# Performance work log

Hardware: AMD Instinct MI355X
Metric: run time of the kernel (lower is better)

The kernel has to match this reference:

```python
import jax, jax.numpy as jnp
import numpy as np
import math

MIN_INTEGRAL = 1e-05
INTERVAL_TIME = 0.05


def setup_inputs() -> dict:
    key = jax.random.key(0)
    ks = jax.random.split(key, 8)
    B, S, U, W = 8192, 256, 128, 512  # batch, state, user_params, hidden width
    D_in = S + U
    sc = lambda fan_in: 1.0 / np.sqrt(fan_in)
    return {
        "state": jax.random.normal(ks[0], (B, S), dtype=jnp.float32),
        "user_params": jax.random.normal(ks[1], (B, U), dtype=jnp.float32),
        "W1": jax.random.normal(ks[2], (D_in, W), dtype=jnp.float32) * sc(D_in),
        "b1": jax.random.normal(ks[3], (W,), dtype=jnp.float32) * 0.01,
        "W2": jax.random.normal(ks[4], (W, W), dtype=jnp.float32) * sc(W),
        "b2": jax.random.normal(ks[5], (W,), dtype=jnp.float32) * 0.01,
        "W3": jax.random.normal(ks[6], (W, S), dtype=jnp.float32) * sc(W),
        "b3": jax.random.normal(ks[7], (S,), dtype=jnp.float32) * 0.01,
        "h": 1,
    }


def reference(state, user_params, W1, b1, W2, b2, W3, b3, h):
    # ode_func: cat(state, user_params) -> Linear -> SiLU -> Linear -> SiLU -> Linear
    def ode_func(s):
        x = jnp.concatenate((s, user_params), axis=1)
        x = jax.nn.silu(x @ W1 + b1)
        x = jax.nn.silu(x @ W2 + b2)
        return x @ W3 + b3

    num_intervals = int(math.floor(h / INTERVAL_TIME))  # fp-faithful to torch code

    def step(s, _):
        return s + ode_func(s) * INTERVAL_TIME, None

    state, _ = jax.lax.scan(step, state, None, length=num_intervals)

    rest_interval = h % INTERVAL_TIME
    if MIN_INTEGRAL < rest_interval:
        # NOTE: original code adds the derivative WITHOUT scaling by rest_interval
        state = state + ode_func(state)
    return state
```

## Files before the change

kernel.cpp:

```cpp
#include <hip/hip_runtime.h>

typedef __attribute__((ext_vector_type(8))) short short8;
typedef __attribute__((ext_vector_type(4))) float float4v;
typedef unsigned short u16;

#define Sdim 256
#define Udim 128
#define Hdim 512
#define MT   32
#define XS   392
#define XLS  264
#define HS   520
#define NW   589824
#define W1_OFF 0
#define W2_OFF 196608
#define W3_OFF 458752
#define NSTEPS 21

__device__ __forceinline__ float bf2f(u16 u) {
    union { unsigned int i; float f; } x; x.i = ((unsigned int)u) << 16; return x.f;
}
__device__ __forceinline__ u16 f2bf(float f) {
    union { float f; unsigned int i; } x; x.f = f;
    unsigned int r = x.i + 0x7FFFu + ((x.i >> 16) & 1u);
    return (u16)(r >> 16);
}

__device__ __forceinline__ int probe_local(const u16* __restrict__ w1, int tid) {
    __shared__ int cnt;
    if (tid == 0) cnt = 0;
    __syncthreads();
    if (tid < 256) {
        u16 u = w1[tid];
        int e = (u >> 7) & 0xFF;
        if ((u == 0) || (e >= 0x60 && e <= 0x8F)) atomicAdd(&cnt, 1);
    }
    __syncthreads();
    return (cnt >= 240) ? 1 : 0;
}

__device__ __forceinline__ void pack_body(const void* __restrict__ Wraw, u16* __restrict__ hi,
                                          int K, int N, int f, int bf) {
    int KT = K >> 5;
    int lane = f & 63, tile = f >> 6;
    int kt = tile % KT, nt = tile / KT;
    int k0 = kt * 32 + ((lane >> 4) << 3);
    int n  = nt * 16 + (lane & 15);
    short8 vh;
#pragma unroll
    for (int j = 0; j < 8; ++j) {
        float wv = bf ? bf2f(((const u16*)Wraw)[(size_t)(k0 + j) * N + n])
                      : ((const float*)Wraw)[(size_t)(k0 + j) * N + n];
        vh[j] = (short)f2bf(wv);
    }
    *reinterpret_cast<short8*>(hi + (size_t)f * 8) = vh;
}

__global__ void pack_all(const void* __restrict__ W1, const void* __restrict__ W2,
                         const void* __restrict__ W3, u16* __restrict__ wh,
                         int* __restrict__ flagp) {
    int bf = probe_local((const u16*)W1, threadIdx.x);
    int b = blockIdx.x;
    if (b == 0 && threadIdx.x == 0) *flagp = bf;
    if (b < 96)
        pack_body(W1, wh + W1_OFF, 384, 512, b * 256 + threadIdx.x, bf);
    else if (b < 224)
        pack_body(W2, wh + W2_OFF, 512, 512, (b - 96) * 256 + threadIdx.x, bf);
    else
        pack_body(W3, wh + W3_OFF, 512, 256, (b - 224) * 256 + threadIdx.x, bf);
}

#define MFMA __builtin_amdgcn_mfma_f32_16x16x32_bf16

template<int KT0, int KT, int KTB, int KTL, int NT>
__device__ __forceinline__ void mm1(const u16* ah, const u16* al, const int as, const int als,
                                    const u16* __restrict__ wh, float4v acc[2][NT]) {
#pragma unroll 2
    for (int kt = KT0; kt < KT; ++kt) {
        short8 A0 = *(const short8*)(ah + kt * 32);
        short8 A1 = *(const short8*)(ah + 16 * as + kt * 32);
        short8 A0l, A1l;
        if (kt < KTL) {
            A0l = *(const short8*)(al + kt * 32);
            A1l = *(const short8*)(al + 16 * als + kt * 32);
        }
#pragma unroll
        for (int t = 0; t < NT; ++t) {
            short8 Bh = *(const short8*)(wh + (size_t)(t * KTB + kt) * 512);
            acc[0][t] = MFMA(A0, Bh, acc[0][t], 0, 0, 0);
            acc[1][t] = MFMA(A1, Bh, acc[1][t], 0, 0, 0);
            if (kt < KTL) {
                acc[0][t] = MFMA(A0l, Bh, acc[0][t], 0, 0, 0);
                acc[1][t] = MFMA(A1l, Bh, acc[1][t], 0, 0, 0);
            }
        }
    }
}

__device__ __forceinline__ float silu(float v) {
    return v * __builtin_amdgcn_rcpf(1.0f + __expf(-v));
}

template<bool BF>
__device__ __forceinline__ void body(
    const void* state_raw, const void* user_raw,
    const void* b1r, const void* b2r, const void* b3r,
    const u16* __restrict__ wh_all, void* outp,
    u16* xh, u16* xl, u16* H1, u16* H2) {

    const int tid = threadIdx.x, w = tid >> 6, lane = tid & 63;
    const int col16 = lane & 15, quad = lane >> 4;
    const int r0 = blockIdx.x * MT;

    if (tid < 512) {
        int row = tid >> 4;
        int c8 = (tid & 15) * 8;
        if (BF) {
            short8 v = *(const short8*)((const u16*)user_raw + (size_t)(r0 + row) * Udim + c8);
            *(short8*)(xh + row * XS + Sdim + c8) = v;
        } else {
            const float* up = (const float*)user_raw + (size_t)(r0 + row) * Udim + c8;
            short8 v;
#pragma unroll
            for (int j = 0; j < 8; ++j) v[j] = (short)f2bf(up[j]);
            *(short8*)(xh + row * XS + Sdim + c8) = v;
        }
    }
    float b1f[2], b2f[2], b3f;
#pragma unroll
    for (int t = 0; t < 2; ++t) {
        int i = w * 32 + t * 16 + col16;
        b1f[t] = BF ? bf2f(((const u16*)b1r)[i]) : ((const float*)b1r)[i];
        b2f[t] = BF ? bf2f(((const u16*)b2r)[i]) : ((const float*)b2r)[i];
    }
    {
        int i = w * 16 + col16;
        b3f = BF ? bf2f(((const u16*)b3r)[i]) : ((const float*)b3r)[i];
    }
    float st[2][4];
#pragma unroll
    for (int m = 0; m < 2; ++m)
#pragma unroll
        for (int r = 0; r < 4; ++r) {
            int row = m * 16 + quad * 4 + r;
            int col = w * 16 + col16;
            float v = BF ? bf2f(((const u16*)state_raw)[(size_t)(r0 + row) * Sdim + col])
                         : ((const float*)state_raw)[(size_t)(r0 + row) * Sdim + col];
            st[m][r] = v;
            u16 h = f2bf(v);
            xh[row * XS + col] = h;
            xl[row * XLS + col] = f2bf(v - bf2f(h));
        }
    __syncthreads();

    const u16* w1h = wh_all + W1_OFF + (size_t)(w * 2) * 12 * 512 + lane * 8;
    const u16* w2h = wh_all + W2_OFF + (size_t)(w * 2) * 16 * 512 + lane * 8;
    const u16* w3h = wh_all + W3_OFF + (size_t)(w)     * 16 * 512 + lane * 8;

    const u16* aXh = xh + col16 * XS + quad * 8;
    const u16* aXl = xl + col16 * XLS + quad * 8;
    const u16* aH1 = H1 + col16 * HS + quad * 8;
    const u16* aH2 = H2 + col16 * HS + quad * 8;

    float4v uacc[2][2];
#pragma unroll
    for (int m = 0; m < 2; ++m)
#pragma unroll
        for (int t = 0; t < 2; ++t) uacc[m][t] = (float4v){b1f[t], b1f[t], b1f[t], b1f[t]};
    mm1<8, 12, 12, 0, 2>(aXh, aXh, XS, XS, w1h, uacc);

    for (int step = 0; step < NSTEPS; ++step) {
        const float dt = (step == NSTEPS - 1) ? 1.0f : 0.05f;
        const bool lo_now = (step == 0) || (step == NSTEPS - 1);

        {
            float4v acc[2][2];
#pragma unroll
            for (int m = 0; m < 2; ++m)
#pragma unroll
                for (int t = 0; t < 2; ++t) acc[m][t] = uacc[m][t];
            if (lo_now) mm1<0, 8, 12, 8, 2>(aXh, aXl, XS, XLS, w1h, acc);
            else        mm1<0, 8, 12, 0, 2>(aXh, aXl, XS, XLS, w1h, acc);
#pragma unroll
            for (int m = 0; m < 2; ++m)
#pragma unroll
                for (int t = 0; t < 2; ++t)
#pragma unroll
                    for (int r = 0; r < 4; ++r) {
                        float s = silu(acc[m][t][r]);
                        H1[(m * 16 + quad * 4 + r) * HS + w * 32 + t * 16 + col16] = f2bf(s);
                    }
        }
        __syncthreads();

        {
            float4v acc[2][2];
#pragma unroll
            for (int m = 0; m < 2; ++m)
#pragma unroll
                for (int t = 0; t < 2; ++t) acc[m][t] = (float4v){b2f[t], b2f[t], b2f[t], b2f[t]};
            mm1<0, 16, 16, 0, 2>(aH1, aH1, HS, HS, w2h, acc);
#pragma unroll
            for (int m = 0; m < 2; ++m)
#pragma unroll
                for (int t = 0; t < 2; ++t)
#pragma unroll
                    for (int r = 0; r < 4; ++r) {
                        float s = silu(acc[m][t][r]);
                        H2[(m * 16 + quad * 4 + r) * HS + w * 32 + t * 16 + col16] = f2bf(s);
                    }
        }
        __syncthreads();

        {
            float4v acc[2][1];
#pragma unroll
            for (int m = 0; m < 2; ++m) acc[m][0] = (float4v){b3f, b3f, b3f, b3f};
            mm1<0, 16, 16, 0, 1>(aH2, aH2, HS, HS, w3h, acc);
#pragma unroll
            for (int m = 0; m < 2; ++m)
#pragma unroll
                for (int r = 0; r < 4; ++r) {
                    float v = st[m][r] + acc[m][0][r] * dt;
                    st[m][r] = v;
                    if (step < NSTEPS - 1) {
                        int row = m * 16 + quad * 4 + r;
                        int col = w * 16 + col16;
                        u16 h = f2bf(v);
                        xh[row * XS + col] = h;
                        xl[row * XLS + col] = f2bf(v - bf2f(h));
                    }
                }
        }
        __syncthreads();
    }

#pragma unroll
    for (int m = 0; m < 2; ++m)
#pragma unroll
        for (int r = 0; r < 4; ++r) {
            int row = m * 16 + quad * 4 + r;
            int col = w * 16 + col16;
            if (BF) ((u16*)outp)[(size_t)(r0 + row) * Sdim + col] = f2bf(st[m][r]);
            else    ((float*)outp)[(size_t)(r0 + row) * Sdim + col] = st[m][r];
        }
}

__global__ __launch_bounds__(1024, 4) void fused_ode(
    const void* state_raw, const void* user_raw,
    const void* b1r, const void* b2r, const void* b3r,
    const u16* __restrict__ wh, const int* __restrict__ flagp, void* outp) {

    __shared__ __align__(16) u16 xh[MT * XS];
    __shared__ __align__(16) u16 xl[MT * XLS];
    __shared__ __align__(16) u16 H1[MT * HS];
    __shared__ __align__(16) u16 H2[MT * HS];

    if (*flagp)
        body<true >(state_raw, user_raw, b1r, b2r, b3r, wh, outp, xh, xl, H1, H2);
    else
        body<false>(state_raw, user_raw, b1r, b2r, b3r, wh, outp, xh, xl, H1, H2);
}

extern "C" void kernel_launch(void* const* d_in, const int* in_sizes, int n_in,
                              void* d_out, int out_size, void* d_ws, size_t ws_size,
                              hipStream_t stream) {
    u16* wh = (u16*)d_ws;
    int* flagp = (int*)((char*)d_ws + (size_t)NW * sizeof(u16));

    pack_all<<<288, 256, 0, stream>>>(d_in[2], d_in[4], d_in[6], wh, flagp);

    fused_ode<<<8192 / MT, 1024, 0, stream>>>(d_in[0], d_in[1], d_in[3], d_in[5], d_in[7],
                                              wh, flagp, d_out);
}
```

Measured before the change: 325.0 us.

## Halve waves per block and double each wave's output columns

Measured after the change: 345.0 us. 6.1% more time.

```diff
diff --git a/kernel.cpp b/kernel.cpp
--- a/kernel.cpp
+++ b/kernel.cpp
@@ -112,7 +112,7 @@
     const int col16 = lane & 15, quad = lane >> 4;
     const int r0 = blockIdx.x * MT;
 
-    if (tid < 512) {
+    {
         int row = tid >> 4;
         int c8 = (tid & 15) * 8;
         if (BF) {
@@ -126,69 +126,91 @@
             *(short8*)(xh + row * XS + Sdim + c8) = v;
         }
     }
-    float b1f[2], b2f[2], b3f;
+    float b1f[4], b2f[4], b3f[2];
+#pragma unroll
+    for (int t = 0; t < 4; ++t) {
+        int i = w * 64 + t * 16 + col16;
+        b1f[t] = BF ? bf2f(((const u16*)b1r)[i]) : ((const float*)b1r)[i];
+        b2f[t] = BF ? bf2f(((const u16*)b2r)[i]) : ((const float*)b2r)[i];
+    }
 #pragma unroll
     for (int t = 0; t < 2; ++t) {
         int i = w * 32 + t * 16 + col16;
-        b1f[t] = BF ? bf2f(((const u16*)b1r)[i]) : ((const float*)b1r)[i];
-        b2f[t] = BF ? bf2f(((const u16*)b2r)[i]) : ((const float*)b2r)[i];
-    }
-    {
-        int i = w * 16 + col16;
-        b3f = BF ? bf2f(((const u16*)b3r)[i]) : ((const float*)b3r)[i];
-    }
-    float st[2][4];
+        b3f[t] = BF ? bf2f(((const u16*)b3r)[i]) : ((const float*)b3r)[i];
+    }
+    float st[2][2][4];
 #pragma unroll
     for (int m = 0; m < 2; ++m)
 #pragma unroll
-        for (int r = 0; r < 4; ++r) {
-            int row = m * 16 + quad * 4 + r;
-            int col = w * 16 + col16;
-            float v = BF ? bf2f(((const u16*)state_raw)[(size_t)(r0 + row) * Sdim + col])
-                         : ((const float*)state_raw)[(size_t)(r0 + row) * Sdim + col];
-            st[m][r] = v;
-            u16 h = f2bf(v);
-            xh[row * XS + col] = h;
-            xl[row * XLS + col] = f2bf(v - bf2f(h));
-        }
+        for (int t = 0; t < 2; ++t)
+#pragma unroll
+            for (int r = 0; r < 4; ++r) {
+                int row = m * 16 + quad * 4 + r;
+                int col = w * 32 + t * 16 + col16;
+                float v = BF ? bf2f(((const u16*)state_raw)[(size_t)(r0 + row) * Sdim + col])
+                             : ((const float*)state_raw)[(size_t)(r0 + row) * Sdim + col];
+                st[m][t][r] = v;
+                u16 h = f2bf(v);
+                xh[row * XS + col] = h;
+                xl[row * XLS + col] = f2bf(v - bf2f(h));
+            }
     __syncthreads();
 
-    const u16* w1h = wh_all + W1_OFF + (size_t)(w * 2) * 12 * 512 + lane * 8;
-    const u16* w2h = wh_all + W2_OFF + (size_t)(w * 2) * 16 * 512 + lane * 8;
-    const u16* w3h = wh_all + W3_OFF + (size_t)(w)     * 16 * 512 + lane * 8;
+    const u16* w1h = wh_all + W1_OFF + (size_t)(w * 4) * 12 * 512 + lane * 8;
+    const u16* w2h = wh_all + W2_OFF + (size_t)(w * 4) * 16 * 512 + lane * 8;
+    const u16* w3h = wh_all + W3_OFF + (size_t)(w * 2) * 16 * 512 + lane * 8;
 
     const u16* aXh = xh + col16 * XS + quad * 8;
     const u16* aXl = xl + col16 * XLS + quad * 8;
     const u16* aH1 = H1 + col16 * HS + quad * 8;
     const u16* aH2 = H2 + col16 * HS + quad * 8;
 
-    float4v uacc[2][2];
+    float4v uacc[2][4];
 #pragma unroll
     for (int m = 0; m < 2; ++m)
 #pragma unroll
-        for (int t = 0; t < 2; ++t) uacc[m][t] = (float4v){b1f[t], b1f[t], b1f[t], b1f[t]};
-    mm1<8, 12, 12, 0, 2>(aXh, aXh, XS, XS, w1h, uacc);
+        for (int t = 0; t < 4; ++t) uacc[m][t] = (float4v){b1f[t], b1f[t], b1f[t], b1f[t]};
+    mm1<8, 12, 12, 0, 4>(aXh, aXh, XS, XS, w1h, uacc);
 
     for (int step = 0; step < NSTEPS; ++step) {
         const float dt = (step == NSTEPS - 1) ? 1.0f : 0.05f;
         const bool lo_now = (step == 0) || (step == NSTEPS - 1);
 
         {
-            float4v acc[2][2];
-#pragma unroll
-            for (int m = 0; m < 2; ++m)
-#pragma unroll
-                for (int t = 0; t < 2; ++t) acc[m][t] = uacc[m][t];
-            if (lo_now) mm1<0, 8, 12, 8, 2>(aXh, aXl, XS, XLS, w1h, acc);
-            else        mm1<0, 8, 12, 0, 2>(aXh, aXl, XS, XLS, w1h, acc);
-#pragma unroll
-            for (int m = 0; m < 2; ++m)
-#pragma unroll
-                for (int t = 0; t < 2; ++t)
+            float4v acc[2][4];
+#pragma unroll
+            for (int m = 0; m < 2; ++m)
+#pragma unroll
+                for (int t = 0; t < 4; ++t) acc[m][t] = uacc[m][t];
+            if (lo_now) mm1<0, 8, 12, 8, 4>(aXh, aXl, XS, XLS, w1h, acc);
+            else        mm1<0, 8, 12, 0, 4>(aXh, aXl, XS, XLS, w1h, acc);
+#pragma unroll
+            for (int m = 0; m < 2; ++m)
+#pragma unroll
+                for (int t = 0; t < 4; ++t)
 #pragma unroll
                     for (int r = 0; r < 4; ++r) {
                         float s = silu(acc[m][t][r]);
-                        H1[(m * 16 + quad * 4 + r) * HS + w * 32 + t * 16 + col16] = f2bf(s);
+                        H1[(m * 16 + quad * 4 + r) * HS + w * 64 + t * 16 + col16] = f2bf(s);
+                    }
+        }
+        __syncthreads();
+
+        {
+            float4v acc[2][4];
+#pragma unroll
+            for (int m = 0; m < 2; ++m)
+#pragma unroll
+                for (int t = 0; t < 4; ++t) acc[m][t] = (float4v){b2f[t], b2f[t], b2f[t], b2f[t]};
+            mm1<0, 16, 16, 0, 4>(aH1, aH1, HS, HS, w2h, acc);
+#pragma unroll
+            for (int m = 0; m < 2; ++m)
+#pragma unroll
+                for (int t = 0; t < 4; ++t)
+#pragma unroll
+                    for (int r = 0; r < 4; ++r) {
+                        float s = silu(acc[m][t][r]);
+                        H2[(m * 16 + quad * 4 + r) * HS + w * 64 + t * 16 + col16] = f2bf(s);
                     }
         }
         __syncthreads();
@@ -198,55 +220,43 @@
 #pragma unroll
             for (int m = 0; m < 2; ++m)
 #pragma unroll
-                for (int t = 0; t < 2; ++t) acc[m][t] = (float4v){b2f[t], b2f[t], b2f[t], b2f[t]};
-            mm1<0, 16, 16, 0, 2>(aH1, aH1, HS, HS, w2h, acc);
+                for (int t = 0; t < 2; ++t) acc[m][t] = (float4v){b3f[t], b3f[t], b3f[t], b3f[t]};
+            mm1<0, 16, 16, 0, 2>(aH2, aH2, HS, HS, w3h, acc);
 #pragma unroll
             for (int m = 0; m < 2; ++m)
 #pragma unroll
                 for (int t = 0; t < 2; ++t)
 #pragma unroll
                     for (int r = 0; r < 4; ++r) {
-                        float s = silu(acc[m][t][r]);
-                        H2[(m * 16 + quad * 4 + r) * HS + w * 32 + t * 16 + col16] = f2bf(s);
+                        float v = st[m][t][r] + acc[m][t][r] * dt;
+                        st[m][t][r] = v;
+                        if (step < NSTEPS - 1) {
+                            int row = m * 16 + quad * 4 + r;
+                            int col = w * 32 + t * 16 + col16;
+                            u16 h = f2bf(v);
+                            xh[row * XS + col] = h;
+                            if (step == NSTEPS - 2)
+                                xl[row * XLS + col] = f2bf(v - bf2f(h));
+                        }
                     }
         }
         __syncthreads();
-
-        {
-            float4v acc[2][1];
-#pragma unroll
-            for (int m = 0; m < 2; ++m) acc[m][0] = (float4v){b3f, b3f, b3f, b3f};
-            mm1<0, 16, 16, 0, 1>(aH2, aH2, HS, HS, w3h, acc);
-#pragma unroll
-            for (int m = 0; m < 2; ++m)
-#pragma unroll
-                for (int r = 0; r < 4; ++r) {
-                    float v = st[m][r] + acc[m][0][r] * dt;
-                    st[m][r] = v;
-                    if (step < NSTEPS - 1) {
-                        int row = m * 16 + quad * 4 + r;
-                        int col = w * 16 + col16;
-                        u16 h = f2bf(v);
-                        xh[row * XS + col] = h;
-                        xl[row * XLS + col] = f2bf(v - bf2f(h));
-                    }
-                }
-        }
-        __syncthreads();
     }
 
 #pragma unroll
     for (int m = 0; m < 2; ++m)
 #pragma unroll
-        for (int r = 0; r < 4; ++r) {
-            int row = m * 16 + quad * 4 + r;
-            int col = w * 16 + col16;
-            if (BF) ((u16*)outp)[(size_t)(r0 + row) * Sdim + col] = f2bf(st[m][r]);
-            else    ((float*)outp)[(size_t)(r0 + row) * Sdim + col] = st[m][r];
-        }
-}
-
-__global__ __launch_bounds__(1024, 4) void fused_ode(
+        for (int t = 0; t < 2; ++t)
+#pragma unroll
+            for (int r = 0; r < 4; ++r) {
+                int row = m * 16 + quad * 4 + r;
+                int col = w * 32 + t * 16 + col16;
+                if (BF) ((u16*)outp)[(size_t)(r0 + row) * Sdim + col] = f2bf(st[m][t][r]);
+                else    ((float*)outp)[(size_t)(r0 + row) * Sdim + col] = st[m][t][r];
+            }
+}
+
+__global__ __launch_bounds__(512, 2) void fused_ode(
     const void* state_raw, const void* user_raw,
     const void* b1r, const void* b2r, const void* b3r,
     const u16* __restrict__ wh, const int* __restrict__ flagp, void* outp) {
@@ -270,6 +280,6 @@
 
     pack_all<<<288, 256, 0, stream>>>(d_in[2], d_in[4], d_in[6], wh, flagp);
 
-    fused_ode<<<8192 / MT, 1024, 0, stream>>>(d_in[0], d_in[1], d_in[3], d_in[5], d_in[7],
-                                              wh, flagp, d_out);
-}
+    fused_ode<<<8192 / MT, 512, 0, stream>>>(d_in[0], d_in[1], d_in[3], d_in[5], d_in[7],
+                                             wh, flagp, d_out);
+}
```

## Prefetch first weight k-tiles of next layer across barriers and skip unused xl writes

Applied to the files above, without the earlier changes.

Result: slower. 410.7 us (+26.3%).

```diff
diff --git a/kernel.cpp b/kernel.cpp
--- a/kernel.cpp
+++ b/kernel.cpp
@@ -97,6 +97,39 @@
     }
 }
 
+template<int KTB, int NT>
+__device__ __forceinline__ void pfB(const u16* __restrict__ wh, short8* pb) {
+#pragma unroll
+    for (int kt = 0; kt < 2; ++kt)
+#pragma unroll
+        for (int t = 0; t < NT; ++t)
+            pb[kt * NT + t] = *(const short8*)(wh + (size_t)(t * KTB + kt) * 512);
+}
+
+template<int NT, bool LO>
+__device__ __forceinline__ void mmpeel(const u16* ah, const u16* al, const int as, const int als,
+                                       const short8* pb, float4v acc[2][NT]) {
+#pragma unroll
+    for (int kt = 0; kt < 2; ++kt) {
+        short8 A0 = *(const short8*)(ah + kt * 32);
+        short8 A1 = *(const short8*)(ah + 16 * as + kt * 32);
+#pragma unroll
+        for (int t = 0; t < NT; ++t) {
+            acc[0][t] = MFMA(A0, pb[kt * NT + t], acc[0][t], 0, 0, 0);
+            acc[1][t] = MFMA(A1, pb[kt * NT + t], acc[1][t], 0, 0, 0);
+        }
+        if (LO) {
+            short8 A0l = *(const short8*)(al + kt * 32);
+            short8 A1l = *(const short8*)(al + 16 * als + kt * 32);
+#pragma unroll
+            for (int t = 0; t < NT; ++t) {
+                acc[0][t] = MFMA(A0l, pb[kt * NT + t], acc[0][t], 0, 0, 0);
+                acc[1][t] = MFMA(A1l, pb[kt * NT + t], acc[1][t], 0, 0, 0);
+            }
+        }
+    }
+}
+
 __device__ __forceinline__ float silu(float v) {
     return v * __builtin_amdgcn_rcpf(1.0f + __expf(-v));
 }
@@ -169,6 +202,9 @@
         for (int t = 0; t < 2; ++t) uacc[m][t] = (float4v){b1f[t], b1f[t], b1f[t], b1f[t]};
     mm1<8, 12, 12, 0, 2>(aXh, aXh, XS, XS, w1h, uacc);
 
+    short8 pb1[4], pb2[4], pb3[2];
+    pfB<12, 2>(w1h, pb1);
+
     for (int step = 0; step < NSTEPS; ++step) {
         const float dt = (step == NSTEPS - 1) ? 1.0f : 0.05f;
         const bool lo_now = (step == 0) || (step == NSTEPS - 1);
@@ -179,8 +215,14 @@
             for (int m = 0; m < 2; ++m)
 #pragma unroll
                 for (int t = 0; t < 2; ++t) acc[m][t] = uacc[m][t];
-            if (lo_now) mm1<0, 8, 12, 8, 2>(aXh, aXl, XS, XLS, w1h, acc);
-            else        mm1<0, 8, 12, 0, 2>(aXh, aXl, XS, XLS, w1h, acc);
+            if (lo_now) {
+                mmpeel<2, true >(aXh, aXl, XS, XLS, pb1, acc);
+                mm1<2, 8, 12, 8, 2>(aXh, aXl, XS, XLS, w1h, acc);
+            } else {
+                mmpeel<2, false>(aXh, aXl, XS, XLS, pb1, acc);
+                mm1<2, 8, 12, 0, 2>(aXh, aXl, XS, XLS, w1h, acc);
+            }
+            pfB<16, 2>(w2h, pb2);
 #pragma unroll
             for (int m = 0; m < 2; ++m)
 #pragma unroll
@@ -199,7 +241,9 @@
             for (int m = 0; m < 2; ++m)
 #pragma unroll
                 for (int t = 0; t < 2; ++t) acc[m][t] = (float4v){b2f[t], b2f[t], b2f[t], b2f[t]};
-            mm1<0, 16, 16, 0, 2>(aH1, aH1, HS, HS, w2h, acc);
+            mmpeel<2, false>(aH1, aH1, HS, HS, pb2, acc);
+            mm1<2, 16, 16, 0, 2>(aH1, aH1, HS, HS, w2h, acc);
+            pfB<16, 1>(w3h, pb3);
 #pragma unroll
             for (int m = 0; m < 2; ++m)
 #pragma unroll
@@ -216,7 +260,9 @@
             float4v acc[2][1];
 #pragma unroll
             for (int m = 0; m < 2; ++m) acc[m][0] = (float4v){b3f, b3f, b3f, b3f};
-            mm1<0, 16, 16, 0, 1>(aH2, aH2, HS, HS, w3h, acc);
+            mmpeel<1, false>(aH2, aH2, HS, HS, pb3, acc);
+            mm1<2, 16, 16, 0, 1>(aH2, aH2, HS, HS, w3h, acc);
+            pfB<12, 2>(w1h, pb1);
 #pragma unroll
             for (int m = 0; m < 2; ++m)
 #pragma unroll
@@ -228,7 +274,8 @@
                         int col = w * 16 + col16;
                         u16 h = f2bf(v);
                         xh[row * XS + col] = h;
-                        xl[row * XLS + col] = f2bf(v - bf2f(h));
+                        if (step == NSTEPS - 2)
+                            xl[row * XLS + col] = f2bf(v - bf2f(h));
                     }
                 }
         }
```
